# Performance work log

Measured on AMD Instinct MI355X. Metric: run time of the kernel, lower is better.

## Reference

```python
import jax, jax.numpy as jnp
import numpy as np

WINDOW_SIZE = 11
SIGMA = 1.5
C1 = 0.01 ** 2
C2 = 0.03 ** 2


def _make_window(channel, dtype=jnp.float32):
    # Faithful to torch `gaussian`: center at window_size/2 (= 5.5 for ws=11)
    x = np.arange(WINDOW_SIZE, dtype=np.float64)
    g = np.exp(-((x - WINDOW_SIZE / 2) ** 2) / (2.0 * SIGMA ** 2))
    g = (g / g.sum()).astype(np.float32)
    w2d = np.outer(g, g)  # (ws, ws)
    w = np.broadcast_to(w2d, (channel, 1, WINDOW_SIZE, WINDOW_SIZE)).copy()
    return jnp.asarray(w, dtype=dtype)


def _dwconv(x, w, channel):
    pad = WINDOW_SIZE // 2
    return jax.lax.conv_general_dilated(
        x, w,
        window_strides=(1, 1),
        padding=[(pad, pad), (pad, pad)],
        dimension_numbers=("NCHW", "OIHW", "NCHW"),
        feature_group_count=channel,
    )


def setup_inputs() -> dict:
    key = jax.random.key(0)
    k1, k2 = jax.random.split(key)
    B, C, H, W = 16, 3, 512, 512
    img1 = jax.random.uniform(k1, (B, C, H, W), dtype=jnp.float32)
    img2 = jax.random.uniform(k2, (B, C, H, W), dtype=jnp.float32)
    return {"img1": img1, "img2": img2}


def reference(img1, img2):
    channel = img1.shape[1]
    window = _make_window(channel, img1.dtype)

    mu1 = _dwconv(img1, window, channel)
    mu2 = _dwconv(img2, window, channel)
    mu1_sq = mu1 * mu1
    mu2_sq = mu2 * mu2
    mu1_mu2 = mu1 * mu2

    sigma1_sq = _dwconv(img1 * img1, window, channel) - mu1_sq
    sigma2_sq = _dwconv(img2 * img2, window, channel) - mu2_sq
    sigma12 = _dwconv(img1 * img2, window, channel) - mu1_mu2

    numerator = (2 * mu1_mu2 + C1) * (2 * sigma12 + C2)
    denominator = (mu1_sq + mu2_sq + C1) * (sigma1_sq + sigma2_sq + C2)
    ssim_map = numerator / denominator
    return jnp.mean(ssim_map)  # size_average=True
```

## Files before the change

kernel.cpp:

```cpp
#include <hip/hip_runtime.h>
#include <cmath>


#define IMG_H 512
#define IMG_W 512
#define STRIPE 32
#define NSTR (IMG_H / STRIPE)
#define NPLANES 48
#define NBLOCKS (NPLANES * NSTR)
#define SSIM_C1 (0.01f * 0.01f)
#define SSIM_C2 (0.03f * 0.03f)

struct W11 { float w[11]; };

__launch_bounds__(512, 4)
__global__ void ssim_main(const float* __restrict__ img1,
                          const float* __restrict__ img2,
                          float* __restrict__ blockSums, W11 wv) {
    __shared__ float tb[2][2][544];
    __shared__ float red[8];

    const int x = threadIdx.x;
    const int bid = blockIdx.x;
    const int plane = bid >> 4;
    const int stripe = bid & (NSTR - 1);
    const int y0 = stripe * STRIPE;
    const size_t base = (size_t)plane * (IMG_H * IMG_W);

    if (x < 10) {
        const int col = (x < 5) ? x : (x + 512);
        tb[0][0][col] = 0.f; tb[0][1][col] = 0.f;
        tb[1][0][col] = 0.f; tb[1][1][col] = 0.f;
    }

    float ring[5][11];
    float acc = 0.f;

    float pa = 0.f, pb = 0.f;
    {
        const int r0 = y0 - 5;
        if (r0 >= 0) {
            pa = img1[base + (size_t)r0 * IMG_W + x];
            pb = img2[base + (size_t)r0 * IMG_W + x];
        }
    }

    int buf = 0;
#pragma unroll 1
    for (int c = 0; c < 4; ++c) {
#pragma unroll
        for (int j = 0; j < 11; ++j) {
            const int i = c * 11 + j;
            if (i < 42) {
                tb[buf][0][x + 5] = pa;
                tb[buf][1][x + 5] = pb;
                pa = 0.f; pb = 0.f;
                const int rn = y0 - 4 + i;
                if (i + 1 < 42 && rn >= 0 && rn < IMG_H) {
                    pa = img1[base + (size_t)rn * IMG_W + x];
                    pb = img2[base + (size_t)rn * IMG_W + x];
                }
                __syncthreads();
                float h0 = 0.f, h1 = 0.f, h2 = 0.f, h3 = 0.f, h4 = 0.f;
#pragma unroll
                for (int k = 0; k < 11; ++k) {
                    const float ta = tb[buf][0][x + k];
                    const float tbv = tb[buf][1][x + k];
                    const float w = wv.w[k];
                    const float wa = w * ta, wb = w * tbv;
                    h0 = fmaf(w, ta, h0);
                    h1 = fmaf(w, tbv, h1);
                    h2 = fmaf(wa, ta, h2);
                    h3 = fmaf(wb, tbv, h3);
                    h4 = fmaf(wa, tbv, h4);
                }
                ring[0][j] = h0; ring[1][j] = h1; ring[2][j] = h2;
                ring[3][j] = h3; ring[4][j] = h4;

                if (i >= 10) {
                    float v0 = 0.f, v1 = 0.f, v2 = 0.f, v3 = 0.f, v4 = 0.f;
#pragma unroll
                    for (int k = 0; k < 11; ++k) {
                        const int s = (j + 1 + k) % 11;
                        const float w = wv.w[k];
                        v0 = fmaf(w, ring[0][s], v0);
                        v1 = fmaf(w, ring[1][s], v1);
                        v2 = fmaf(w, ring[2][s], v2);
                        v3 = fmaf(w, ring[3][s], v3);
                        v4 = fmaf(w, ring[4][s], v4);
                    }
                    const float mu11 = v0 * v0;
                    const float mu22 = v1 * v1;
                    const float mu12 = v0 * v1;
                    const float num = (2.f * mu12 + SSIM_C1) *
                                      (2.f * (v4 - mu12) + SSIM_C2);
                    const float den = (mu11 + mu22 + SSIM_C1) *
                                      ((v2 - mu11) + (v3 - mu22) + SSIM_C2);
                    acc += num / den;
                }
                buf ^= 1;
            }
        }
    }

#pragma unroll
    for (int off = 32; off >= 1; off >>= 1)
        acc += __shfl_down(acc, off, 64);
    const int wave = x >> 6, lane = x & 63;
    if (lane == 0) red[wave] = acc;
    __syncthreads();
    if (x == 0) {
        float s = 0.f;
#pragma unroll
        for (int k = 0; k < 8; ++k) s += red[k];
        blockSums[bid] = s;
    }
}

__global__ void ssim_reduce(const float* __restrict__ bs,
                            float* __restrict__ out) {
    __shared__ double red[4];
    const int t = threadIdx.x;
    double a = 0.0;
    for (int idx = t; idx < NBLOCKS; idx += 256) a += (double)bs[idx];
#pragma unroll
    for (int off = 32; off >= 1; off >>= 1)
        a += __shfl_down(a, off, 64);
    const int wave = t >> 6, lane = t & 63;
    if (lane == 0) red[wave] = a;
    __syncthreads();
    if (t == 0) {
        const double s = red[0] + red[1] + red[2] + red[3];
        out[0] = (float)(s / (double)((double)NPLANES * IMG_H * IMG_W));
    }
}

extern "C" void kernel_launch(void* const* d_in, const int* in_sizes, int n_in,
                              void* d_out, int out_size, void* d_ws, size_t ws_size,
                              hipStream_t stream) {
    const float* img1 = (const float*)d_in[0];
    const float* img2 = (const float*)d_in[1];
    float* out = (float*)d_out;
    float* bs = (float*)d_ws;

    W11 wv;
    double g[11], s = 0.0;
    for (int i = 0; i < 11; ++i) {
        const double d = (double)i - 5.5;
        g[i] = exp(-(d * d) / (2.0 * 1.5 * 1.5));
        s += g[i];
    }
    for (int i = 0; i < 11; ++i) wv.w[i] = (float)(g[i] / s);

    ssim_main<<<NBLOCKS, 512, 0, stream>>>(img1, img2, bs, wv);
    ssim_reduce<<<1, 256, 0, stream>>>(bs, out);
}
```

Before: 167.3 us.

## Merge squared-sum channels, interleave LDS rows as float2, use fast reciprocal

The kernel now tracks four filtered quantities instead of five by convolving x²+y² as one term, since only the sum of the two squared-image filters enters the denominator. The shared row buffer is interleaved as float2 so each tap needs one 64-bit LDS read instead of two scalar reads. The final division becomes a hardware approximate reciprocal folded into an fma. Together these cut ALU work, register use for the ring and LDS instruction count. The cost is slightly different rounding from the merged squares and the approximate reciprocal.

```diff
diff --git a/kernel.cpp b/kernel.cpp
--- a/kernel.cpp
+++ b/kernel.cpp
@@ -17,7 +17,7 @@
 __global__ void ssim_main(const float* __restrict__ img1,
                           const float* __restrict__ img2,
                           float* __restrict__ blockSums, W11 wv) {
-    __shared__ float tb[2][2][544];
+    __shared__ float2 tb[2][528];
     __shared__ float red[8];
 
     const int x = threadIdx.x;
@@ -29,11 +29,11 @@
 
     if (x < 10) {
         const int col = (x < 5) ? x : (x + 512);
-        tb[0][0][col] = 0.f; tb[0][1][col] = 0.f;
-        tb[1][0][col] = 0.f; tb[1][1][col] = 0.f;
+        tb[0][col] = make_float2(0.f, 0.f);
+        tb[1][col] = make_float2(0.f, 0.f);
     }
 
-    float ring[5][11];
+    float rA[11], rB[11], rS[11], rP[11];
     float acc = 0.f;
 
     float pa = 0.f, pb = 0.f;
@@ -52,8 +52,7 @@
         for (int j = 0; j < 11; ++j) {
             const int i = c * 11 + j;
             if (i < 42) {
-                tb[buf][0][x + 5] = pa;
-                tb[buf][1][x + 5] = pb;
+                tb[buf][x + 5] = make_float2(pa, pb);
                 pa = 0.f; pb = 0.f;
                 const int rn = y0 - 4 + i;
                 if (i + 1 < 42 && rn >= 0 && rn < IMG_H) {
@@ -61,42 +60,39 @@
                     pb = img2[base + (size_t)rn * IMG_W + x];
                 }
                 __syncthreads();
-                float h0 = 0.f, h1 = 0.f, h2 = 0.f, h3 = 0.f, h4 = 0.f;
+                float h0 = 0.f, h1 = 0.f, h2 = 0.f, h3 = 0.f;
 #pragma unroll
                 for (int k = 0; k < 11; ++k) {
-                    const float ta = tb[buf][0][x + k];
-                    const float tbv = tb[buf][1][x + k];
+                    const float2 t = tb[buf][x + k];
                     const float w = wv.w[k];
-                    const float wa = w * ta, wb = w * tbv;
-                    h0 = fmaf(w, ta, h0);
-                    h1 = fmaf(w, tbv, h1);
-                    h2 = fmaf(wa, ta, h2);
-                    h3 = fmaf(wb, tbv, h3);
-                    h4 = fmaf(wa, tbv, h4);
+                    const float sq = fmaf(t.y, t.y, t.x * t.x);
+                    const float pr = t.x * t.y;
+                    h0 = fmaf(w, t.x, h0);
+                    h1 = fmaf(w, t.y, h1);
+                    h2 = fmaf(w, sq, h2);
+                    h3 = fmaf(w, pr, h3);
                 }
-                ring[0][j] = h0; ring[1][j] = h1; ring[2][j] = h2;
-                ring[3][j] = h3; ring[4][j] = h4;
+                rA[j] = h0; rB[j] = h1; rS[j] = h2; rP[j] = h3;
 
                 if (i >= 10) {
-                    float v0 = 0.f, v1 = 0.f, v2 = 0.f, v3 = 0.f, v4 = 0.f;
+                    float vA = 0.f, vB = 0.f, vS = 0.f, vP = 0.f;
 #pragma unroll
                     for (int k = 0; k < 11; ++k) {
                         const int s = (j + 1 + k) % 11;
                         const float w = wv.w[k];
-                        v0 = fmaf(w, ring[0][s], v0);
-                        v1 = fmaf(w, ring[1][s], v1);
-                        v2 = fmaf(w, ring[2][s], v2);
-                        v3 = fmaf(w, ring[3][s], v3);
-                        v4 = fmaf(w, ring[4][s], v4);
+                        vA = fmaf(w, rA[s], vA);
+                        vB = fmaf(w, rB[s], vB);
+                        vS = fmaf(w, rS[s], vS);
+                        vP = fmaf(w, rP[s], vP);
                     }
-                    const float mu11 = v0 * v0;
-                    const float mu22 = v1 * v1;
-                    const float mu12 = v0 * v1;
-                    const float num = (2.f * mu12 + SSIM_C1) *
-                                      (2.f * (v4 - mu12) + SSIM_C2);
-                    const float den = (mu11 + mu22 + SSIM_C1) *
-                                      ((v2 - mu11) + (v3 - mu22) + SSIM_C2);
-                    acc += num / den;
+                    const float mu11 = vA * vA;
+                    const float mu22 = vB * vB;
+                    const float mu12 = vA * vB;
+                    const float num = fmaf(2.f, mu12, SSIM_C1) *
+                                      fmaf(2.f, vP - mu12, SSIM_C2);
+                    const float d1  = mu11 + mu22;
+                    const float den = (d1 + SSIM_C1) * ((vS - d1) + SSIM_C2);
+                    acc = fmaf(num, __builtin_amdgcn_rcpf(den), acc);
                 }
                 buf ^= 1;
             }
```

New measurement: 153.6 us. -8.2%, faster.
